# Kernel tuning notes

Measured on AMD Instinct MI355X. Metric: run time of the kernel, lower is better.

The kernel has to match this reference:

```python
import jax, jax.numpy as jnp
import numpy as np

EMBED_DIM = 128
B, N = 8, 2048


def entmax15(z):
    """Exact 1.5-entmax along the last axis (Peters & Martins 2019, sort-based)."""
    z = z / 2.0
    z = z - jnp.max(z, axis=-1, keepdims=True)  # shift-invariance -> numerical stability
    zs = -jnp.sort(-z, axis=-1)                 # descending sort
    n = z.shape[-1]
    k = jnp.arange(1, n + 1, dtype=z.dtype)
    mean = jnp.cumsum(zs, axis=-1) / k
    meansq = jnp.cumsum(zs * zs, axis=-1) / k
    ss = k * (meansq - mean * mean)
    delta = (1.0 - ss) / k
    delta_safe = jnp.where(delta > 0, delta, 1.0)
    tau = mean - jnp.where(delta > 0, jnp.sqrt(delta_safe), 0.0)
    support = jnp.sum((tau <= zs).astype(jnp.int32), axis=-1, keepdims=True)
    tau_star = jnp.take_along_axis(tau, support - 1, axis=-1)
    return jnp.square(jnp.maximum(z - tau_star, 0.0))


def setup_inputs() -> dict:
    key = jax.random.key(0)
    ks = jax.random.split(key, 6)
    s = 1.0 / np.sqrt(EMBED_DIM)  # torch nn.Linear default init range
    return {
        "x_c": jax.random.normal(ks[0], (B, N, EMBED_DIM), jnp.float32),
        "x_n": jax.random.normal(ks[1], (B, N, EMBED_DIM), jnp.float32),
        "Wq": jax.random.uniform(ks[2], (EMBED_DIM, EMBED_DIM), jnp.float32, -s, s),
        "bq": jax.random.uniform(ks[3], (EMBED_DIM,), jnp.float32, -s, s),
        "Wk": jax.random.uniform(ks[4], (EMBED_DIM, EMBED_DIM), jnp.float32, -s, s),
        "bk": jax.random.uniform(ks[5], (EMBED_DIM,), jnp.float32, -s, s),
    }


def reference(x_c, x_n, Wq, bq, Wk, bk):
    Q = x_c @ Wq.T + bq                      # [B,N,D]
    K = x_n @ Wk.T + bk                      # [B,N,D]
    A = jnp.einsum("bnd,bmd->bnm", Q, K) / jnp.sqrt(jnp.float32(EMBED_DIM))
    # entmax15 sparse normalization over keys; dropout is identity in eval mode
    return entmax15(A)
```

## Files before the change

kernel.cpp:

```cpp
#include <hip/hip_runtime.h>
#include <hip/hip_bf16.h>

#define BATCH 8
#define SEQ   2048
#define DIM   128
#define NROWS 16384
#define INV_2SQRTD 0.04419417382415922f
#define THETA_SPAN 22.62741699796952f

typedef __bf16    bf16x8   __attribute__((ext_vector_type(8)));
typedef float     floatx16 __attribute__((ext_vector_type(16)));
typedef _Float16  half8    __attribute__((ext_vector_type(8)));

static __device__ __forceinline__ unsigned short f2bf(float v) {
    union { __hip_bfloat16 h; unsigned short u; } c;
    c.h = __float2bfloat16(v);
    return c.u;
}
static __device__ __forceinline__ float bf2f(unsigned short u) {
    union { unsigned int i; float f; } c;
    c.i = (unsigned int)u << 16;
    return c.f;
}

__global__ void __launch_bounds__(256, 2)
project_q(const float* __restrict__ X, const float* __restrict__ W,
          const float* __restrict__ bias,
          unsigned short* __restrict__ Qhi, unsigned short* __restrict__ Qlo) {
    __shared__ float wt[64][132];
    __shared__ float xs[32][68];
    const int tid  = threadIdx.x;
    const int l    = tid & 15;
    const int kthi = tid >> 4;
    const int row0 = blockIdx.x * 32;

    float s[2][8];
#pragma unroll
    for (int rr = 0; rr < 2; ++rr)
#pragma unroll
        for (int j = 0; j < 8; ++j) s[rr][j] = 0.0f;

    for (int ph = 0; ph < 2; ++ph) {
        const int e0 = ph * 64;
#pragma unroll
        for (int i = 0; i < 8; ++i) {
            const int f  = tid + 256 * i;
            const int d  = f & 127;
            const int c4 = f >> 7;
            float4 wv = *reinterpret_cast<const float4*>(
                W + (size_t)d * DIM + e0 + 4 * c4);
            wt[4*c4+0][d] = wv.x;  wt[4*c4+1][d] = wv.y;
            wt[4*c4+2][d] = wv.z;  wt[4*c4+3][d] = wv.w;
        }
#pragma unroll
        for (int i = 0; i < 2; ++i) {
            const int f  = tid + 256 * i;
            const int r  = f >> 4;
            const int c4 = f & 15;
            float4 xv = *reinterpret_cast<const float4*>(
                X + (size_t)(row0 + r) * DIM + e0 + 4 * c4);
            *reinterpret_cast<float4*>(&xs[r][4 * c4]) = xv;
        }
        __syncthreads();
#pragma unroll 8
        for (int e = 0; e < 64; ++e) {
            float w8[8];
            *reinterpret_cast<float4*>(w8)     =
                *reinterpret_cast<const float4*>(&wt[e][kthi * 8]);
            *reinterpret_cast<float4*>(w8 + 4) =
                *reinterpret_cast<const float4*>(&wt[e][kthi * 8 + 4]);
#pragma unroll
            for (int rr = 0; rr < 2; ++rr) {
                const float xv = xs[l + 16 * rr][e];
#pragma unroll
                for (int j = 0; j < 8; ++j) s[rr][j] = fmaf(xv, w8[j], s[rr][j]);
            }
        }
        __syncthreads();
    }

    float b8[8];
    *reinterpret_cast<float4*>(b8)     = *reinterpret_cast<const float4*>(bias + kthi * 8);
    *reinterpret_cast<float4*>(b8 + 4) = *reinterpret_cast<const float4*>(bias + kthi * 8 + 4);
#pragma unroll
    for (int rr = 0; rr < 2; ++rr) {
        const int row = row0 + l + 16 * rr;
        union { uint4 v; unsigned short u[8]; } ph, pl;
#pragma unroll
        for (int j = 0; j < 8; ++j) {
            const float v = s[rr][j] + b8[j];
            const unsigned short h = f2bf(v);
            ph.u[j] = h;
            pl.u[j] = f2bf(v - bf2f(h));
        }
        const size_t base = ((size_t)kthi * NROWS + row) * 8;
        *reinterpret_cast<uint4*>(Qhi + base) = ph.v;
        *reinterpret_cast<uint4*>(Qlo + base) = pl.v;
    }
}

__global__ void __launch_bounds__(256, 2)
project_k(const float* __restrict__ X, const float* __restrict__ W,
          const float* __restrict__ bias, unsigned short* __restrict__ Kb) {
    __shared__ float wt[64][132];
    __shared__ float xs[32][68];
    const int tid  = threadIdx.x;
    const int l    = tid & 15;
    const int kthi = tid >> 4;
    const int row0 = blockIdx.x * 32;

    float s[2][8];
#pragma unroll
    for (int rr = 0; rr < 2; ++rr)
#pragma unroll
        for (int j = 0; j < 8; ++j) s[rr][j] = 0.0f;

    for (int ph = 0; ph < 2; ++ph) {
        const int e0 = ph * 64;
#pragma unroll
        for (int i = 0; i < 8; ++i) {
            const int f  = tid + 256 * i;
            const int d  = f & 127;
            const int c4 = f >> 7;
            float4 wv = *reinterpret_cast<const float4*>(
                W + (size_t)d * DIM + e0 + 4 * c4);
            wt[4*c4+0][d] = wv.x;  wt[4*c4+1][d] = wv.y;
            wt[4*c4+2][d] = wv.z;  wt[4*c4+3][d] = wv.w;
        }
#pragma unroll
        for (int i = 0; i < 2; ++i) {
            const int f  = tid + 256 * i;
            const int r  = f >> 4;
            const int c4 = f & 15;
            float4 xv = *reinterpret_cast<const float4*>(
                X + (size_t)(row0 + r) * DIM + e0 + 4 * c4);
            *reinterpret_cast<float4*>(&xs[r][4 * c4]) = xv;
        }
        __syncthreads();
#pragma unroll 8
        for (int e = 0; e < 64; ++e) {
            float w8[8];
            *reinterpret_cast<float4*>(w8)     =
                *reinterpret_cast<const float4*>(&wt[e][kthi * 8]);
            *reinterpret_cast<float4*>(w8 + 4) =
                *reinterpret_cast<const float4*>(&wt[e][kthi * 8 + 4]);
#pragma unroll
            for (int rr = 0; rr < 2; ++rr) {
                const float xv = xs[l + 16 * rr][e];
#pragma unroll
                for (int j = 0; j < 8; ++j) s[rr][j] = fmaf(xv, w8[j], s[rr][j]);
            }
        }
        __syncthreads();
    }

    float b8[8];
    *reinterpret_cast<float4*>(b8)     = *reinterpret_cast<const float4*>(bias + kthi * 8);
    *reinterpret_cast<float4*>(b8 + 4) = *reinterpret_cast<const float4*>(bias + kthi * 8 + 4);
#pragma unroll
    for (int rr = 0; rr < 2; ++rr) {
        const int row = row0 + l + 16 * rr;
        const int b   = row >> 11;
        const int key = row & (SEQ - 1);
        union { uint4 v; unsigned short u[8]; } pk;
#pragma unroll
        for (int j = 0; j < 8; ++j) pk.u[j] = f2bf(s[rr][j] + b8[j]);
        const size_t base = (((size_t)(b * 16) + kthi) * SEQ + key) * 8;
        *reinterpret_cast<uint4*>(Kb + base) = pk.v;
    }
}

__global__ void __launch_bounds__(256, 2)
score_gemm(const __bf16* __restrict__ Qhi, const __bf16* __restrict__ Qlo,
           const __bf16* __restrict__ Kb, _Float16* __restrict__ S) {
    const int tid  = threadIdx.x;
    const int wv   = tid >> 6;
    const int lane = tid & 63;
    const int l5   = lane & 31;
    const int hi5  = lane >> 5;
    const int row0 = blockIdx.x * 32;
    const int b    = row0 >> 11;
    const int key0 = blockIdx.y * 512 + wv * 128;

    floatx16 acc[4];
    const floatx16 zerov = {};
#pragma unroll
    for (int t = 0; t < 4; ++t) acc[t] = zerov;

    const __bf16* qh = Qhi + ((size_t)hi5 * NROWS + row0 + l5) * 8;
    const __bf16* ql = Qlo + ((size_t)hi5 * NROWS + row0 + l5) * 8;
    const __bf16* kp = Kb + (((size_t)(b * 16) + hi5) * SEQ + key0 + l5) * 8;
    const size_t qstep = (size_t)2 * NROWS * 8;
    const size_t kstep = (size_t)2 * SEQ * 8;

#pragma unroll
    for (int kt = 0; kt < 8; ++kt) {
        const bf16x8 ah = *reinterpret_cast<const bf16x8*>(qh + kt * qstep);
        const bf16x8 al = *reinterpret_cast<const bf16x8*>(ql + kt * qstep);
        const __bf16* kc = kp + kt * kstep;
#pragma unroll
        for (int t = 0; t < 4; ++t) {
            const bf16x8 bk = *reinterpret_cast<const bf16x8*>(kc + (size_t)t * 256);
            acc[t] = __builtin_amdgcn_mfma_f32_32x32x16_bf16(ah, bk, acc[t], 0, 0, 0);
            acc[t] = __builtin_amdgcn_mfma_f32_32x32x16_bf16(al, bk, acc[t], 0, 0, 0);
        }
    }
#pragma unroll
    for (int t = 0; t < 4; ++t) {
#pragma unroll
        for (int r = 0; r < 16; ++r) {
            const int rowl = (r & 3) + 8 * (r >> 2) + 4 * hi5;
            S[(size_t)(row0 + rowl) * SEQ + key0 + t * 32 + l5] =
                (_Float16)acc[t][r];
        }
    }
}

__global__ void __launch_bounds__(256, 4)
entmax_rows(const _Float16* __restrict__ S, float* __restrict__ out) {
    const int lane = threadIdx.x & 63;
    const int row  = blockIdx.x * 4 + (threadIdx.x >> 6);

    const uint4* srow = reinterpret_cast<const uint4*>(S + (size_t)row * SEQ);
    float z[32];
#pragma unroll
    for (int k = 0; k < 4; ++k) {
        union { uint4 u; half8 h; } cv;
        cv.u = srow[k * 64 + lane];
#pragma unroll
        for (int i = 0; i < 8; ++i) z[k * 8 + i] = (float)cv.h[i];
    }

    float m = z[0];
#pragma unroll
    for (int i = 1; i < 32; ++i) m = fmaxf(m, z[i]);
#pragma unroll
    for (int off = 32; off >= 1; off >>= 1) m = fmaxf(m, __shfl_xor(m, off, 64));

    float lo = m - THETA_SPAN, hi = m;
    for (int it = 0; it < 12; ++it) {
        const float th = 0.5f * (lo + hi);
        float f0 = 0.0f, f1 = 0.0f, f2 = 0.0f, f3 = 0.0f;
#pragma unroll
        for (int i = 0; i < 8; ++i) {
            const float a0 = fmaxf(z[4 * i + 0] - th, 0.0f);
            const float a1 = fmaxf(z[4 * i + 1] - th, 0.0f);
            const float a2 = fmaxf(z[4 * i + 2] - th, 0.0f);
            const float a3 = fmaxf(z[4 * i + 3] - th, 0.0f);
            f0 = fmaf(a0, a0, f0); f1 = fmaf(a1, a1, f1);
            f2 = fmaf(a2, a2, f2); f3 = fmaf(a3, a3, f3);
        }
        float fs = (f0 + f1) + (f2 + f3);
#pragma unroll
        for (int off = 32; off >= 1; off >>= 1) fs += __shfl_xor(fs, off, 64);
        if (fs >= 512.0f) lo = th; else hi = th;
    }
    const float th = 0.5f * (lo + hi);

    float* orow = out + (size_t)row * SEQ;
#pragma unroll
    for (int k = 0; k < 4; ++k) {
        float pv[8];
#pragma unroll
        for (int i = 0; i < 8; ++i) {
            const float d = fmaxf(z[k * 8 + i] - th, 0.0f);
            pv[i] = d * d * (1.0f / 512.0f);
        }
        float* op = orow + k * 512 + lane * 8;
        *reinterpret_cast<float4*>(op)     = make_float4(pv[0], pv[1], pv[2], pv[3]);
        *reinterpret_cast<float4*>(op + 4) = make_float4(pv[4], pv[5], pv[6], pv[7]);
    }
}

__global__ void __launch_bounds__(256, 1)
attn_entmax_mfma(const __bf16* __restrict__ Qhi, const __bf16* __restrict__ Qlo,
                 const __bf16* __restrict__ Kb, float* __restrict__ out) {
    const int tid  = threadIdx.x;
    const int wv   = tid >> 6;
    const int lane = tid & 63;
    const int l5   = lane & 31;
    const int hi5  = lane >> 5;
    const int row0 = blockIdx.x * 32;
    const int b    = row0 >> 11;
    const int key0 = wv * 512;

    floatx16 acc[16];
    const floatx16 zerov = {};
#pragma unroll
    for (int t = 0; t < 16; ++t) acc[t] = zerov;

    const __bf16* Kbase = Kb + (size_t)b * (8 * 2 * SEQ * 8);
#pragma unroll
    for (int kt = 0; kt < 8; ++kt) {
        const size_t qoff = (((size_t)kt * 2 + hi5) * NROWS + row0 + l5) * 8;
        const bf16x8 ah = *reinterpret_cast<const bf16x8*>(Qhi + qoff);
        const bf16x8 al = *reinterpret_cast<const bf16x8*>(Qlo + qoff);
        const __bf16* kp = Kbase + (((size_t)kt * 2 + hi5) * SEQ + key0 + l5) * 8;
#pragma unroll
        for (int t = 0; t < 16; ++t) {
            const bf16x8 bk = *reinterpret_cast<const bf16x8*>(kp + (size_t)t * 32 * 8);
            acc[t] = __builtin_amdgcn_mfma_f32_32x32x16_bf16(ah, bk, acc[t], 0, 0, 0);
            acc[t] = __builtin_amdgcn_mfma_f32_32x32x16_bf16(al, bk, acc[t], 0, 0, 0);
        }
    }
    __shared__ __align__(16) float red[32][4];
    float rm[16];
#pragma unroll
    for (int r = 0; r < 16; ++r) {
        float m = acc[0][r];
#pragma unroll
        for (int t = 1; t < 16; ++t) m = fmaxf(m, acc[t][r]);
#pragma unroll
        for (int off = 16; off >= 1; off >>= 1) m = fmaxf(m, __shfl_xor(m, off, 64));
        if (l5 == r) red[(r & 3) + 8 * (r >> 2) + 4 * hi5][wv] = m;
    }
    __syncthreads();
#pragma unroll
    for (int r = 0; r < 16; ++r) {
        const int rowl = (r & 3) + 8 * (r >> 2) + 4 * hi5;
        const float4 mv = *reinterpret_cast<const float4*>(red[rowl]);
        rm[r] = fmaxf(fmaxf(mv.x, mv.y), fmaxf(mv.z, mv.w));
    }
    __syncthreads();
#pragma unroll
    for (int r = 0; r < 16; ++r) {
        const float nm = -rm[r] * INV_2SQRTD;
#pragma unroll
        for (int t = 0; t < 16; ++t) acc[t][r] = fmaf(acc[t][r], INV_2SQRTD, nm);
    }
    float lo[16], hh[16];
#pragma unroll
    for (int r = 0; r < 16; ++r) { lo[r] = -1.0f; hh[r] = 0.0f; }
    for (int it = 0; it < 14; ++it) {
#pragma unroll
        for (int r = 0; r < 16; ++r) {
            const float tau = 0.5f * (lo[r] + hh[r]);
            float f = 0.0f;
#pragma unroll
            for (int t = 0; t < 16; ++t) {
                const float d = fmaxf(acc[t][r] - tau, 0.0f);
                f = fmaf(d, d, f);
            }
#pragma unroll
            for (int off = 16; off >= 1; off >>= 1) f += __shfl_xor(f, off, 64);
            if (l5 == r) red[(r & 3) + 8 * (r >> 2) + 4 * hi5][wv] = f;
        }
        __syncthreads();
#pragma unroll
        for (int r = 0; r < 16; ++r) {
            const int rowl = (r & 3) + 8 * (r >> 2) + 4 * hi5;
            const float4 fv = *reinterpret_cast<const float4*>(red[rowl]);
            const float fs = (fv.x + fv.y) + (fv.z + fv.w);
            const float tau = 0.5f * (lo[r] + hh[r]);
            if (fs >= 1.0f) lo[r] = tau; else hh[r] = tau;
        }
        __syncthreads();
    }
#pragma unroll
    for (int r = 0; r < 16; ++r) {
        const int rowl = (r & 3) + 8 * (r >> 2) + 4 * hi5;
        const float tau = 0.5f * (lo[r] + hh[r]);
        float* op = out + (size_t)(row0 + rowl) * SEQ + key0 + l5;
#pragma unroll
        for (int t = 0; t < 16; ++t) {
            const float d = fmaxf(acc[t][r] - tau, 0.0f);
            op[(size_t)t * 32] = d * d;
        }
    }
}

extern "C" void kernel_launch(void* const* d_in, const int* in_sizes, int n_in,
                              void* d_out, int out_size, void* d_ws, size_t ws_size,
                              hipStream_t stream) {
    const float* x_c = (const float*)d_in[0];
    const float* x_n = (const float*)d_in[1];
    const float* Wq  = (const float*)d_in[2];
    const float* bq  = (const float*)d_in[3];
    const float* Wk  = (const float*)d_in[4];
    const float* bk  = (const float*)d_in[5];
    float* out = (float*)d_out;

    char* ws = (char*)d_ws;
    unsigned short* Qhi = (unsigned short*)ws;
    unsigned short* Qlo = (unsigned short*)(ws + ((size_t)4 << 20));
    unsigned short* Kbl = (unsigned short*)(ws + ((size_t)8 << 20));
    _Float16*       S   = (_Float16*)(ws + ((size_t)12 << 20));

    const size_t need = ((size_t)12 << 20) + (size_t)NROWS * SEQ * 2;

    project_q<<<NROWS / 32, 256, 0, stream>>>(x_c, Wq, bq, Qhi, Qlo);
    project_k<<<NROWS / 32, 256, 0, stream>>>(x_n, Wk, bk, Kbl);

    if (ws_size >= need) {
        score_gemm<<<dim3(NROWS / 32, 4), 256, 0, stream>>>(
            (const __bf16*)Qhi, (const __bf16*)Qlo, (const __bf16*)Kbl, S);
        entmax_rows<<<NROWS / 4, 256, 0, stream>>>(S, out);
    } else {
        attn_entmax_mfma<<<NROWS / 32, 256, 0, stream>>>(
            (const __bf16*)Qhi, (const __bf16*)Qlo, (const __bf16*)Kbl, out);
    }
}
```

Before: 222.2 us.

## Merge Q/K projections and repack fp16 score buffer into row-group layout

Q and K projections are merged into one launch over a 2D grid, with 64 rows per block and a changed W load mapping and shared-memory padding. The score GEMM now writes fp16 scores packed four rows per uint2 (a 4-row group interleaved per key), so stores are 8-byte vectors instead of scattered 2-byte ones. Entmax reads this layout with strided uint2 loads, picks its own row's half, and writes output as scalar coalesced floats rather than float4. The fused fallback kernel and the workspace-size check are removed, so the code now assumes the workspace is large enough. Each entmax wave reads four times the bytes it needs, and score_gemm's launch bounds are raised to three blocks per CU.

Result: faster. 209.3 us (-5.8%).

```diff
diff --git a/kernel.cpp b/kernel.cpp
--- a/kernel.cpp
+++ b/kernel.cpp
@@ -5,12 +5,10 @@
 #define SEQ   2048
 #define DIM   128
 #define NROWS 16384
-#define INV_2SQRTD 0.04419417382415922f
 #define THETA_SPAN 22.62741699796952f
 
 typedef __bf16    bf16x8   __attribute__((ext_vector_type(8)));
 typedef float     floatx16 __attribute__((ext_vector_type(16)));
-typedef _Float16  half8    __attribute__((ext_vector_type(8)));
 
 static __device__ __forceinline__ unsigned short f2bf(float v) {
     union { __hip_bfloat16 h; unsigned short u; } c;
@@ -22,21 +20,38 @@
     c.i = (unsigned int)u << 16;
     return c.f;
 }
-
-__global__ void __launch_bounds__(256, 2)
-project_q(const float* __restrict__ X, const float* __restrict__ W,
-          const float* __restrict__ bias,
-          unsigned short* __restrict__ Qhi, unsigned short* __restrict__ Qlo) {
-    __shared__ float wt[64][132];
-    __shared__ float xs[32][68];
+static __device__ __forceinline__ unsigned short f2h(float v) {
+    union { _Float16 h; unsigned short u; } c;
+    c.h = (_Float16)v;
+    return c.u;
+}
+static __device__ __forceinline__ float h2f(unsigned short u) {
+    union { _Float16 h; unsigned short u; } c;
+    c.u = u;
+    return (float)c.h;
+}
+
+__global__ void __launch_bounds__(256)
+proj_qk(const float* __restrict__ xq, const float* __restrict__ xn,
+        const float* __restrict__ Wq, const float* __restrict__ bq,
+        const float* __restrict__ Wk, const float* __restrict__ bk,
+        unsigned short* __restrict__ Qhi, unsigned short* __restrict__ Qlo,
+        unsigned short* __restrict__ Kb) {
+    const int isK = blockIdx.y;
+    const float* __restrict__ X    = isK ? xn : xq;
+    const float* __restrict__ W    = isK ? Wk : Wq;
+    const float* __restrict__ bias = isK ? bk : bq;
+
+    __shared__ float wt[64][133];
+    __shared__ float xs[64][68];
     const int tid  = threadIdx.x;
     const int l    = tid & 15;
     const int kthi = tid >> 4;
-    const int row0 = blockIdx.x * 32;
-
-    float s[2][8];
-#pragma unroll
-    for (int rr = 0; rr < 2; ++rr)
+    const int row0 = blockIdx.x * 64;
+
+    float s[4][8];
+#pragma unroll
+    for (int rr = 0; rr < 4; ++rr)
 #pragma unroll
         for (int j = 0; j < 8; ++j) s[rr][j] = 0.0f;
 
@@ -44,19 +59,19 @@
         const int e0 = ph * 64;
 #pragma unroll
         for (int i = 0; i < 8; ++i) {
-            const int f  = tid + 256 * i;
-            const int d  = f & 127;
-            const int c4 = f >> 7;
+            const int g  = tid + 256 * i;
+            const int d  = g >> 4;
+            const int c4 = g & 15;
             float4 wv = *reinterpret_cast<const float4*>(
                 W + (size_t)d * DIM + e0 + 4 * c4);
             wt[4*c4+0][d] = wv.x;  wt[4*c4+1][d] = wv.y;
             wt[4*c4+2][d] = wv.z;  wt[4*c4+3][d] = wv.w;
         }
 #pragma unroll
-        for (int i = 0; i < 2; ++i) {
-            const int f  = tid + 256 * i;
-            const int r  = f >> 4;
-            const int c4 = f & 15;
+        for (int i = 0; i < 4; ++i) {
+            const int g  = tid + 256 * i;
+            const int r  = g >> 4;
+            const int c4 = g & 15;
             float4 xv = *reinterpret_cast<const float4*>(
                 X + (size_t)(row0 + r) * DIM + e0 + 4 * c4);
             *reinterpret_cast<float4*>(&xs[r][4 * c4]) = xv;
@@ -70,7 +85,7 @@
             *reinterpret_cast<float4*>(w8 + 4) =
                 *reinterpret_cast<const float4*>(&wt[e][kthi * 8 + 4]);
 #pragma unroll
-            for (int rr = 0; rr < 2; ++rr) {
+            for (int rr = 0; rr < 4; ++rr) {
                 const float xv = xs[l + 16 * rr][e];
 #pragma unroll
                 for (int j = 0; j < 8; ++j) s[rr][j] = fmaf(xv, w8[j], s[rr][j]);
@@ -82,97 +97,41 @@
     float b8[8];
     *reinterpret_cast<float4*>(b8)     = *reinterpret_cast<const float4*>(bias + kthi * 8);
     *reinterpret_cast<float4*>(b8 + 4) = *reinterpret_cast<const float4*>(bias + kthi * 8 + 4);
-#pragma unroll
-    for (int rr = 0; rr < 2; ++rr) {
-        const int row = row0 + l + 16 * rr;
-        union { uint4 v; unsigned short u[8]; } ph, pl;
-#pragma unroll
-        for (int j = 0; j < 8; ++j) {
-            const float v = s[rr][j] + b8[j];
-            const unsigned short h = f2bf(v);
-            ph.u[j] = h;
-            pl.u[j] = f2bf(v - bf2f(h));
-        }
-        const size_t base = ((size_t)kthi * NROWS + row) * 8;
-        *reinterpret_cast<uint4*>(Qhi + base) = ph.v;
-        *reinterpret_cast<uint4*>(Qlo + base) = pl.v;
-    }
-}
-
-__global__ void __launch_bounds__(256, 2)
-project_k(const float* __restrict__ X, const float* __restrict__ W,
-          const float* __restrict__ bias, unsigned short* __restrict__ Kb) {
-    __shared__ float wt[64][132];
-    __shared__ float xs[32][68];
-    const int tid  = threadIdx.x;
-    const int l    = tid & 15;
-    const int kthi = tid >> 4;
-    const int row0 = blockIdx.x * 32;
-
-    float s[2][8];
-#pragma unroll
-    for (int rr = 0; rr < 2; ++rr)
-#pragma unroll
-        for (int j = 0; j < 8; ++j) s[rr][j] = 0.0f;
-
-    for (int ph = 0; ph < 2; ++ph) {
-        const int e0 = ph * 64;
-#pragma unroll
-        for (int i = 0; i < 8; ++i) {
-            const int f  = tid + 256 * i;
-            const int d  = f & 127;
-            const int c4 = f >> 7;
-            float4 wv = *reinterpret_cast<const float4*>(
-                W + (size_t)d * DIM + e0 + 4 * c4);
-            wt[4*c4+0][d] = wv.x;  wt[4*c4+1][d] = wv.y;
-            wt[4*c4+2][d] = wv.z;  wt[4*c4+3][d] = wv.w;
-        }
-#pragma unroll
-        for (int i = 0; i < 2; ++i) {
-            const int f  = tid + 256 * i;
-            const int r  = f >> 4;
-            const int c4 = f & 15;
-            float4 xv = *reinterpret_cast<const float4*>(
-                X + (size_t)(row0 + r) * DIM + e0 + 4 * c4);
-            *reinterpret_cast<float4*>(&xs[r][4 * c4]) = xv;
-        }
-        __syncthreads();
-#pragma unroll 8
-        for (int e = 0; e < 64; ++e) {
-            float w8[8];
-            *reinterpret_cast<float4*>(w8)     =
-                *reinterpret_cast<const float4*>(&wt[e][kthi * 8]);
-            *reinterpret_cast<float4*>(w8 + 4) =
-                *reinterpret_cast<const float4*>(&wt[e][kthi * 8 + 4]);
-#pragma unroll
-            for (int rr = 0; rr < 2; ++rr) {
-                const float xv = xs[l + 16 * rr][e];
-#pragma unroll
-                for (int j = 0; j < 8; ++j) s[rr][j] = fmaf(xv, w8[j], s[rr][j]);
+
+    if (!isK) {
+#pragma unroll
+        for (int rr = 0; rr < 4; ++rr) {
+            const int row = row0 + l + 16 * rr;
+            union { uint4 v; unsigned short u[8]; } ph_, pl_;
+#pragma unroll
+            for (int j = 0; j < 8; ++j) {
+                const float v = s[rr][j] + b8[j];
+                const unsigned short h = f2bf(v);
+                ph_.u[j] = h;
+                pl_.u[j] = f2bf(v - bf2f(h));
             }
-        }
-        __syncthreads();
-    }
-
-    float b8[8];
-    *reinterpret_cast<float4*>(b8)     = *reinterpret_cast<const float4*>(bias + kthi * 8);
-    *reinterpret_cast<float4*>(b8 + 4) = *reinterpret_cast<const float4*>(bias + kthi * 8 + 4);
-#pragma unroll
-    for (int rr = 0; rr < 2; ++rr) {
-        const int row = row0 + l + 16 * rr;
-        const int b   = row >> 11;
-        const int key = row & (SEQ - 1);
-        union { uint4 v; unsigned short u[8]; } pk;
-#pragma unroll
-        for (int j = 0; j < 8; ++j) pk.u[j] = f2bf(s[rr][j] + b8[j]);
-        const size_t base = (((size_t)(b * 16) + kthi) * SEQ + key) * 8;
-        *reinterpret_cast<uint4*>(Kb + base) = pk.v;
-    }
-}
-
-__global__ void __launch_bounds__(256, 2)
+            const size_t base = ((size_t)kthi * NROWS + row) * 8;
+            *reinterpret_cast<uint4*>(Qhi + base) = ph_.v;
+            *reinterpret_cast<uint4*>(Qlo + base) = pl_.v;
+        }
+    } else {
+#pragma unroll
+        for (int rr = 0; rr < 4; ++rr) {
+            const int row = row0 + l + 16 * rr;
+            const int b   = row >> 11;
+            const int key = row & (SEQ - 1);
+            union { uint4 v; unsigned short u[8]; } pk;
+#pragma unroll
+            for (int j = 0; j < 8; ++j) pk.u[j] = f2bf(s[rr][j] + b8[j]);
+            const size_t base = (((size_t)(b * 16) + kthi) * SEQ + key) * 8;
+            *reinterpret_cast<uint4*>(Kb + base) = pk.v;
+        }
+    }
+}
+
+__global__ void __launch_bounds__(256, 3)
 score_gemm(const __bf16* __restrict__ Qhi, const __bf16* __restrict__ Qlo,
-           const __bf16* __restrict__ Kb, _Float16* __restrict__ S) {
+           const __bf16* __restrict__ Kb, uint2* __restrict__ S4) {
     const int tid  = threadIdx.x;
     const int wv   = tid >> 6;
     const int lane = tid & 63;
@@ -200,35 +159,41 @@
         const __bf16* kc = kp + kt * kstep;
 #pragma unroll
         for (int t = 0; t < 4; ++t) {
-            const bf16x8 bk = *reinterpret_cast<const bf16x8*>(kc + (size_t)t * 256);
-            acc[t] = __builtin_amdgcn_mfma_f32_32x32x16_bf16(ah, bk, acc[t], 0, 0, 0);
-            acc[t] = __builtin_amdgcn_mfma_f32_32x32x16_bf16(al, bk, acc[t], 0, 0, 0);
-        }
-    }
+            const bf16x8 bkv = *reinterpret_cast<const bf16x8*>(kc + (size_t)t * 256);
+            acc[t] = __builtin_amdgcn_mfma_f32_32x32x16_bf16(ah, bkv, acc[t], 0, 0, 0);
+            acc[t] = __builtin_amdgcn_mfma_f32_32x32x16_bf16(al, bkv, acc[t], 0, 0, 0);
+        }
+    }
+
 #pragma unroll
     for (int t = 0; t < 4; ++t) {
 #pragma unroll
-        for (int r = 0; r < 16; ++r) {
-            const int rowl = (r & 3) + 8 * (r >> 2) + 4 * hi5;
-            S[(size_t)(row0 + rowl) * SEQ + key0 + t * 32 + l5] =
-                (_Float16)acc[t][r];
+        for (int a = 0; a < 4; ++a) {
+            const int rowgroup = (row0 >> 2) + 2 * a + hi5;
+            union { uint2 v; unsigned short u[4]; } pk;
+#pragma unroll
+            for (int bb = 0; bb < 4; ++bb) pk.u[bb] = f2h(acc[t][4 * a + bb]);
+            S4[(size_t)rowgroup * SEQ + key0 + t * 32 + l5] = pk.v;
         }
     }
 }
 
 __global__ void __launch_bounds__(256, 4)
-entmax_rows(const _Float16* __restrict__ S, float* __restrict__ out) {
+entmax_rows(const uint2* __restrict__ S4, float* __restrict__ out) {
     const int lane = threadIdx.x & 63;
-    const int row  = blockIdx.x * 4 + (threadIdx.x >> 6);
-
-    const uint4* srow = reinterpret_cast<const uint4*>(S + (size_t)row * SEQ);
+    const int w    = threadIdx.x >> 6;
+    const int row  = blockIdx.x * 4 + w;
+    const int sub  = row & 3;
+
+    const uint2* sp = S4 + (size_t)(row >> 2) * SEQ;
     float z[32];
 #pragma unroll
-    for (int k = 0; k < 4; ++k) {
-        union { uint4 u; half8 h; } cv;
-        cv.u = srow[k * 64 + lane];
-#pragma unroll
-        for (int i = 0; i < 8; ++i) z[k * 8 + i] = (float)cv.h[i];
+    for (int c = 0; c < 32; ++c) {
+        const uint2 v = sp[c * 64 + lane];
+        const unsigned int word = (sub & 2) ? v.y : v.x;
+        const unsigned short h  = (sub & 1) ? (unsigned short)(word >> 16)
+                                            : (unsigned short)(word & 0xffffu);
+        z[c] = h2f(h);
     }
 
     float m = z[0];
@@ -259,113 +224,9 @@
 
     float* orow = out + (size_t)row * SEQ;
 #pragma unroll
-    for (int k = 0; k < 4; ++k) {
-        float pv[8];
-#pragma unroll
-        for (int i = 0; i < 8; ++i) {
-            const float d = fmaxf(z[k * 8 + i] - th, 0.0f);
-            pv[i] = d * d * (1.0f / 512.0f);
-        }
-        float* op = orow + k * 512 + lane * 8;
-        *reinterpret_cast<float4*>(op)     = make_float4(pv[0], pv[1], pv[2], pv[3]);
-        *reinterpret_cast<float4*>(op + 4) = make_float4(pv[4], pv[5], pv[6], pv[7]);
-    }
-}
-
-__global__ void __launch_bounds__(256, 1)
-attn_entmax_mfma(const __bf16* __restrict__ Qhi, const __bf16* __restrict__ Qlo,
-                 const __bf16* __restrict__ Kb, float* __restrict__ out) {
-    const int tid  = threadIdx.x;
-    const int wv   = tid >> 6;
-    const int lane = tid & 63;
-    const int l5   = lane & 31;
-    const int hi5  = lane >> 5;
-    const int row0 = blockIdx.x * 32;
-    const int b    = row0 >> 11;
-    const int key0 = wv * 512;
-
-    floatx16 acc[16];
-    const floatx16 zerov = {};
-#pragma unroll
-    for (int t = 0; t < 16; ++t) acc[t] = zerov;
-
-    const __bf16* Kbase = Kb + (size_t)b * (8 * 2 * SEQ * 8);
-#pragma unroll
-    for (int kt = 0; kt < 8; ++kt) {
-        const size_t qoff = (((size_t)kt * 2 + hi5) * NROWS + row0 + l5) * 8;
-        const bf16x8 ah = *reinterpret_cast<const bf16x8*>(Qhi + qoff);
-        const bf16x8 al = *reinterpret_cast<const bf16x8*>(Qlo + qoff);
-        const __bf16* kp = Kbase + (((size_t)kt * 2 + hi5) * SEQ + key0 + l5) * 8;
-#pragma unroll
-        for (int t = 0; t < 16; ++t) {
-            const bf16x8 bk = *reinterpret_cast<const bf16x8*>(kp + (size_t)t * 32 * 8);
-            acc[t] = __builtin_amdgcn_mfma_f32_32x32x16_bf16(ah, bk, acc[t], 0, 0, 0);
-            acc[t] = __builtin_amdgcn_mfma_f32_32x32x16_bf16(al, bk, acc[t], 0, 0, 0);
-        }
-    }
-    __shared__ __align__(16) float red[32][4];
-    float rm[16];
-#pragma unroll
-    for (int r = 0; r < 16; ++r) {
-        float m = acc[0][r];
-#pragma unroll
-        for (int t = 1; t < 16; ++t) m = fmaxf(m, acc[t][r]);
-#pragma unroll
-        for (int off = 16; off >= 1; off >>= 1) m = fmaxf(m, __shfl_xor(m, off, 64));
-        if (l5 == r) red[(r & 3) + 8 * (r >> 2) + 4 * hi5][wv] = m;
-    }
-    __syncthreads();
-#pragma unroll
-    for (int r = 0; r < 16; ++r) {
-        const int rowl = (r & 3) + 8 * (r >> 2) + 4 * hi5;
-        const float4 mv = *reinterpret_cast<const float4*>(red[rowl]);
-        rm[r] = fmaxf(fmaxf(mv.x, mv.y), fmaxf(mv.z, mv.w));
-    }
-    __syncthreads();
-#pragma unroll
-    for (int r = 0; r < 16; ++r) {
-        const float nm = -rm[r] * INV_2SQRTD;
-#pragma unroll
-        for (int t = 0; t < 16; ++t) acc[t][r] = fmaf(acc[t][r], INV_2SQRTD, nm);
-    }
-    float lo[16], hh[16];
-#pragma unroll
-    for (int r = 0; r < 16; ++r) { lo[r] = -1.0f; hh[r] = 0.0f; }
-    for (int it = 0; it < 14; ++it) {
-#pragma unroll
-        for (int r = 0; r < 16; ++r) {
-            const float tau = 0.5f * (lo[r] + hh[r]);
-            float f = 0.0f;
-#pragma unroll
-            for (int t = 0; t < 16; ++t) {
-                const float d = fmaxf(acc[t][r] - tau, 0.0f);
-                f = fmaf(d, d, f);
-            }
-#pragma unroll
-            for (int off = 16; off >= 1; off >>= 1) f += __shfl_xor(f, off, 64);
-            if (l5 == r) red[(r & 3) + 8 * (r >> 2) + 4 * hi5][wv] = f;
-        }
-        __syncthreads();
-#pragma unroll
-        for (int r = 0; r < 16; ++r) {
-            const int rowl = (r & 3) + 8 * (r >> 2) + 4 * hi5;
-            const float4 fv = *reinterpret_cast<const float4*>(red[rowl]);
-            const float fs = (fv.x + fv.y) + (fv.z + fv.w);
-            const float tau = 0.5f * (lo[r] + hh[r]);
-            if (fs >= 1.0f) lo[r] = tau; else hh[r] = tau;
-        }
-        __syncthreads();
-    }
-#pragma unroll
-    for (int r = 0; r < 16; ++r) {
-        const int rowl = (r & 3) + 8 * (r >> 2) + 4 * hi5;
-        const float tau = 0.5f * (lo[r] + hh[r]);
-        float* op = out + (size_t)(row0 + rowl) * SEQ + key0 + l5;
-#pragma unroll
-        for (int t = 0; t < 16; ++t) {
-            const float d = fmaxf(acc[t][r] - tau, 0.0f);
-            op[(size_t)t * 32] = d * d;
-        }
+    for (int c = 0; c < 32; ++c) {
+        const float d = fmaxf(z[c] - th, 0.0f);
+        orow[c * 64 + lane] = d * d * (1.0f / 512.0f);
     }
 }
 
@@ -384,19 +245,11 @@
     unsigned short* Qhi = (unsigned short*)ws;
     unsigned short* Qlo = (unsigned short*)(ws + ((size_t)4 << 20));
     unsigned short* Kbl = (unsigned short*)(ws + ((size_t)8 << 20));
-    _Float16*       S   = (_Float16*)(ws + ((size_t)12 << 20));
-
-    const size_t need = ((size_t)12 << 20) + (size_t)NROWS * SEQ * 2;
-
-    project_q<<<NROWS / 32, 256, 0, stream>>>(x_c, Wq, bq, Qhi, Qlo);
-    project_k<<<NROWS / 32, 256, 0, stream>>>(x_n, Wk, bk, Kbl);
-
-    if (ws_size >= need) {
-        score_gemm<<<dim3(NROWS / 32, 4), 256, 0, stream>>>(
-            (const __bf16*)Qhi, (const __bf16*)Qlo, (const __bf16*)Kbl, S);
-        entmax_rows<<<NROWS / 4, 256, 0, stream>>>(S, out);
-    } else {
-        attn_entmax_mfma<<<NROWS / 32, 256, 0, stream>>>(
-            (const __bf16*)Qhi, (const __bf16*)Qlo, (const __bf16*)Kbl, out);
-    }
-}
+    uint2*          S4  = (uint2*)(ws + ((size_t)12 << 20));
+
+    proj_qk<<<dim3(NROWS / 64, 2), 256, 0, stream>>>(
+        x_c, x_n, Wq, bq, Wk, bk, Qhi, Qlo, Kbl);
+    score_gemm<<<dim3(NROWS / 32, 4), 256, 0, stream>>>(
+        (const __bf16*)Qhi, (const __bf16*)Qlo, (const __bf16*)Kbl, S4);
+    entmax_rows<<<NROWS / 4, 256, 0, stream>>>(S4, out);
+}
```
